# Kernel tuning notes

Measured on AMD Instinct MI355X. Metric: run time of the kernel, lower is better.

Reference implementation:

```python
import jax, jax.numpy as jnp
import numpy as np

N_HEADS = 16
INPUT_DIM = 1024
EMBED_DIM = 1024
KEY_DIM = EMBED_DIM // N_HEADS  # 64, val_dim == key_dim
BATCH = 4
SEQ = 2048


def _uniform(key, shape, bound):
    return jax.random.uniform(key, shape, jnp.float32, -bound, bound)


def setup_inputs() -> dict:
    key = jax.random.key(0)
    kq, k1, k2, k3, k4 = jax.random.split(key, 5)
    stdv_k = 1.0 / np.sqrt(KEY_DIM)
    stdv_e = 1.0 / np.sqrt(EMBED_DIM)
    return {
        "q": jax.random.normal(kq, (BATCH, SEQ, INPUT_DIM), jnp.float32),
        "W_query": _uniform(k1, (N_HEADS, INPUT_DIM, KEY_DIM), stdv_k),
        "W_key": _uniform(k2, (N_HEADS, INPUT_DIM, KEY_DIM), stdv_k),
        "W_val": _uniform(k3, (N_HEADS, INPUT_DIM, KEY_DIM), stdv_k),
        "W_out": _uniform(k4, (N_HEADS, KEY_DIM, EMBED_DIM), stdv_e),
    }


def reference(q, W_query, W_key, W_val, W_out):
    # Self-attention: h = q. Project per head: [H, B, S, dk]
    norm = 1.0 / np.sqrt(KEY_DIM)
    Q = jnp.einsum("bsd,hdk->hbsk", q, W_query)
    K = jnp.einsum("bsd,hdk->hbsk", q, W_key)
    V = jnp.einsum("bsd,hdv->hbsv", q, W_val)
    # compatibility: [H, B, S_q, S_k]
    scores = norm * jnp.einsum("hbqk,hbnk->hbqn", Q, K)
    attn = jax.nn.softmax(scores, axis=-1)
    heads = jnp.einsum("hbqn,hbnv->hbqv", attn, V)
    # combine heads with per-head output projection: [B, S, E]
    out = jnp.einsum("hbqv,hve->bqe", heads, W_out)
    return out
```

## Files before the change

kernel.cpp:

```cpp
#include <hip/hip_runtime.h>
#include <hip/hip_bf16.h>
#include <stdint.h>
#include <math.h>

#define BATCH 4
#define SEQ   2048
#define NHEAD 16
#define DIM   1024
#define DKV   64
#define MTOT  (BATCH*SEQ)

typedef __attribute__((ext_vector_type(8))) short  bf16x8;
typedef __attribute__((ext_vector_type(4))) float  f32x4;
typedef unsigned short u16;
typedef unsigned int   u32;
typedef __attribute__((ext_vector_type(4))) u16 u16x4;
typedef __attribute__((ext_vector_type(2))) u32 u32x2;
typedef __attribute__((ext_vector_type(4))) u32 u32x4;

#define QSCALE 0.18033688011112042f
#define THR    8.0f

__device__ __forceinline__ u16 f2bf(float f) {
  __hip_bfloat16 h = __float2bfloat16(f);
  u16 r;
  __builtin_memcpy(&r, &h, 2);
  return r;
}
__device__ __forceinline__ u32 pkbf(float lo, float hi) {
  __hip_bfloat162 h = __float22bfloat162_rn(float2{lo, hi});
  u32 r;
  __builtin_memcpy(&r, &h, 4);
  return r;
}

__device__ __forceinline__ void gload_lds16(const void* g, void* l) {
  __builtin_amdgcn_global_load_lds((u32 __attribute__((address_space(1)))*)(g),
                                   (u32 __attribute__((address_space(3)))*)(l),
                                   16, 0, 0);
}


__global__ void k_cvt_q(const float* __restrict__ src, u16* __restrict__ dst) {
  const int i = (blockIdx.x * 256 + threadIdx.x) * 4;
  float4 v = *(const float4*)(src + i);
  u32x2 o;
  o[0] = pkbf(v.x, v.y); o[1] = pkbf(v.z, v.w);
  *(u32x2*)(dst + i) = o;
}

__global__ void k_cvt_wproj(const float* __restrict__ w, u16* __restrict__ wt) {
  const int idx = blockIdx.x * 256 + threadIdx.x;
  const int n = idx >> 10, d = idx & 1023;
  wt[idx] = f2bf(w[((n >> 6) << 16) + (d << 6) + (n & 63)]);
}

__global__ void k_cvt_wout(const float* __restrict__ w, u16* __restrict__ wt) {
  const int idx = blockIdx.x * 256 + threadIdx.x;
  const int e = idx >> 10, hv = idx & 1023;
  wt[idx] = f2bf(w[(hv << 10) + e]);
}


template<int MODE>
__device__ __forceinline__ void gemm2(u16* __restrict__ sm,
                                      const u16* __restrict__ A, const u16* __restrict__ Bt,
                                      void* __restrict__ Cp, int m0, int n0) {
  const int tid = threadIdx.x, wid = tid >> 6, lane = tid & 63;
  const int g = lane >> 4, li = lane & 15;
  const int wm = wid >> 1, wn = wid & 1;

  const int c0 = wid * 128 + lane, c1 = c0 + 64;
  const int s0 = (c0 * 8) ^ (((c0 >> 3) & 7) << 3);
  const int s1 = (c1 * 8) ^ (((c1 >> 3) & 7) << 3);
  const int cB = tid;
  const int sB = (cB * 8) ^ (((cB >> 3) & 7) << 3);
  const u16* As0 = A  + (size_t)(m0 + (s0 >> 5)) * DIM + (s0 & 31);
  const u16* As1 = A  + (size_t)(m0 + (s1 >> 5)) * DIM + (s1 & 31);
  const u16* Bs  = Bt + (size_t)(n0 + (sB >> 5)) * DIM + (sB & 31);
  u16* dA0 = sm + wid * 1024;
  u16* dA1 = sm + wid * 1024 + 512;
  u16* dB  = sm + 32768 + wid * 512;

#define SA2(t, ks, tb) do { \
    gload_lds16(As0 + (t) * 64 + (ks) * 32, dA0 + (tb) * 16384 + (ks) * 8192); \
    gload_lds16(As1 + (t) * 64 + (ks) * 32, dA1 + (tb) * 16384 + (ks) * 8192); } while (0)
#define SB2(t, ks, tb) \
    gload_lds16(Bs + (t) * 64 + (ks) * 32, dB + (tb) * 8192 + (ks) * 4096)

  const int vx = ((li >> 1) & 7) << 3;
  const int a_rd = (((wm * 64 + li) * 32) + g * 8) ^ vx;
  const int b_rd = (((wn * 64 + li) * 32) + g * 8) ^ vx;

  f32x4 acc[4][4] = {};

  SA2(0, 0, 0); SB2(0, 0, 0);
  SA2(0, 1, 0); SB2(0, 1, 0);
  SA2(1, 0, 1); SB2(1, 0, 1);
  asm volatile("s_waitcnt vmcnt(6)" ::: "memory");
  __builtin_amdgcn_s_barrier();

#pragma unroll 2
  for (int kt = 0; kt < 16; ++kt) {
    const int cur = kt & 1, t1 = (kt + 1) & 15, t2 = (kt + 2) & 15;
    const u16* pa = sm + cur * 16384 + a_rd;
    const u16* pb = sm + 32768 + cur * 8192 + b_rd;
    bf16x8 af[2], bfq[4];

#pragma unroll
    for (int j = 0; j < 4; ++j) bfq[j] = *(const bf16x8*)(pb + j * 512);
    af[0] = *(const bf16x8*)(pa);
    af[1] = *(const bf16x8*)(pa + 512);
    SA2(t1, 1, cur ^ 1);
    __builtin_amdgcn_s_barrier();
    __builtin_amdgcn_s_setprio(1);
#pragma unroll
    for (int i = 0; i < 2; ++i)
#pragma unroll
      for (int j = 0; j < 4; ++j)
        acc[i][j] = __builtin_amdgcn_mfma_f32_16x16x32_bf16(af[i], bfq[j], acc[i][j], 0, 0, 0);
    __builtin_amdgcn_s_setprio(0);
    __builtin_amdgcn_s_barrier();

    af[0] = *(const bf16x8*)(pa + 2 * 512);
    af[1] = *(const bf16x8*)(pa + 3 * 512);
    SB2(t1, 1, cur ^ 1);
    __builtin_amdgcn_s_barrier();
    __builtin_amdgcn_s_setprio(1);
#pragma unroll
    for (int i = 0; i < 2; ++i)
#pragma unroll
      for (int j = 0; j < 4; ++j)
        acc[i + 2][j] = __builtin_amdgcn_mfma_f32_16x16x32_bf16(af[i], bfq[j], acc[i + 2][j], 0, 0, 0);
    __builtin_amdgcn_s_setprio(0);
    asm volatile("s_waitcnt vmcnt(3)" ::: "memory");
    __builtin_amdgcn_s_barrier();

#pragma unroll
    for (int j = 0; j < 4; ++j) bfq[j] = *(const bf16x8*)(pb + 4096 + j * 512);
    af[0] = *(const bf16x8*)(pa + 8192);
    af[1] = *(const bf16x8*)(pa + 8192 + 512);
    SA2(t2, 0, cur);
    __builtin_amdgcn_s_barrier();
    __builtin_amdgcn_s_setprio(1);
#pragma unroll
    for (int i = 0; i < 2; ++i)
#pragma unroll
      for (int j = 0; j < 4; ++j)
        acc[i][j] = __builtin_amdgcn_mfma_f32_16x16x32_bf16(af[i], bfq[j], acc[i][j], 0, 0, 0);
    __builtin_amdgcn_s_setprio(0);
    __builtin_amdgcn_s_barrier();

    af[0] = *(const bf16x8*)(pa + 8192 + 2 * 512);
    af[1] = *(const bf16x8*)(pa + 8192 + 3 * 512);
    SB2(t2, 0, cur);
    __builtin_amdgcn_s_barrier();
    __builtin_amdgcn_s_setprio(1);
#pragma unroll
    for (int i = 0; i < 2; ++i)
#pragma unroll
      for (int j = 0; j < 4; ++j)
        acc[i + 2][j] = __builtin_amdgcn_mfma_f32_16x16x32_bf16(af[i], bfq[j], acc[i + 2][j], 0, 0, 0);
    __builtin_amdgcn_s_setprio(0);
    asm volatile("s_waitcnt vmcnt(3)" ::: "memory");
    __builtin_amdgcn_s_barrier();
  }
#undef SA2
#undef SB2

#pragma unroll
  for (int i = 0; i < 4; ++i)
#pragma unroll
    for (int j = 0; j < 4; ++j) {
      const int col = n0 + wn * 64 + j * 16 + li;
      if (MODE == 3) {
        const size_t rowb = (size_t)(m0 + wm * 64 + i * 16 + g * 4) + 4 * g - 12 * (i & 1);
        u32x2 w;
        w[0] = pkbf(acc[i][j][0], acc[i][j][1]);
        w[1] = pkbf(acc[i][j][2], acc[i][j][3]);
        *(u32x2*)((u16*)Cp + (size_t)col * MTOT + rowb) = w;
      } else if (MODE == 1) {
#pragma unroll
        for (int r = 0; r < 4; ++r) {
          const size_t row = (size_t)(m0 + wm * 64 + i * 16 + g * 4 + r);
          ((float*)Cp)[row * DIM + col] = acc[i][j][r];
        }
      } else {
#pragma unroll
        for (int r = 0; r < 4; ++r) {
          const size_t row = (size_t)(m0 + wm * 64 + i * 16 + g * 4 + r);
          float v = acc[i][j][r];
          if (MODE == 2) v *= QSCALE;
          ((u16*)Cp)[row * DIM + col] = f2bf(v);
        }
      }
    }
}

__global__ __launch_bounds__(512, 2)
void k_gemm_qkv2(const u16* __restrict__ A, const u16* __restrict__ wq,
                 const u16* __restrict__ wk, const u16* __restrict__ wv,
                 u16* __restrict__ Qo, u16* __restrict__ Ko, u16* __restrict__ Vto) {
  __shared__ u16 sm[49152];
  const int m0 = blockIdx.x * 256;
  const int yt = blockIdx.y;
  const int wsel = yt >> 3;
  const int n0 = (yt & 7) * 128;
  if (wsel == 0)      gemm2<2>(sm, A, wq, Qo,  m0, n0);
  else if (wsel == 1) gemm2<0>(sm, A, wk, Ko,  m0, n0);
  else                gemm2<3>(sm, A, wv, Vto, m0, n0);
}

__global__ __launch_bounds__(512, 2)
void k_gemm_out2(const u16* __restrict__ A, const u16* __restrict__ Bt, float* __restrict__ C) {
  __shared__ u16 sm[49152];
  gemm2<1>(sm, A, Bt, C, blockIdx.x * 256, blockIdx.y * 128);
}


#define KB 64
#define NT (SEQ/KB)

__global__ __launch_bounds__(512, 8)
void k_attn(const u16* __restrict__ Q, const u16* __restrict__ K,
            const u16* __restrict__ Vt, u16* __restrict__ O) {
  const int qt = blockIdx.x, bh = blockIdx.y;
  const int b = bh >> 4, h = bh & 15;
  const int q0 = qt * 128;
  const int tid = threadIdx.x, wid = tid >> 6, lane = tid & 63;
  const int g = lane >> 4, li = lane & 15;

  __shared__ u16 kl[2][KB * 64];
  __shared__ u16 vl[2][KB * 64];

  const size_t rb = (size_t)b * SEQ;
  const int hc = h * DKV;

  bf16x8 qf0, qf1;
  {
    const u16* qp = Q + (rb + q0 + wid * 16 + li) * DIM + hc;
    qf0 = *(const bf16x8*)(qp + g * 8);
    qf1 = *(const bf16x8*)(qp + 32 + g * 8);
  }

  bf16x8 ones;
#pragma unroll
  for (int j = 0; j < 8; ++j) ones[j] = (short)0x3F80;

  float mrun = -1e30f, lrun = 0.f;
  f32x4 o[4] = {};

  const int r8   = lane >> 3;
  const int swz  = ((lane & 7) ^ r8) * 8;
  const int srow = wid * 8 + r8;

  gload_lds16(K  + (rb + srow) * DIM + hc + swz,          &kl[0][wid * 512]);
  gload_lds16(Vt + (size_t)(hc + srow) * MTOT + rb + swz, &vl[0][wid * 512]);

  for (int it = 0; it < NT; ++it) {
    const int cur = it & 1;
    __syncthreads();

    if (it + 1 < NT) {
      const int n1 = (it + 1) * KB;
      gload_lds16(K  + (rb + n1 + srow) * DIM + hc + swz,          &kl[cur ^ 1][wid * 512]);
      gload_lds16(Vt + (size_t)(hc + srow) * MTOT + rb + n1 + swz, &vl[cur ^ 1][wid * 512]);
    }

    const u16* kb = kl[cur];
    const u16* vb = vl[cur];
    const int sw = (li & 7) << 3;

    f32x4 s[4];
    __builtin_amdgcn_s_setprio(1);
#pragma unroll
    for (int t = 0; t < 4; ++t) {
      const int row = t * 16 + li;
      bf16x8 kf0 = *(const bf16x8*)(kb + row * 64 + ((g * 8) ^ sw));
      bf16x8 kf1 = *(const bf16x8*)(kb + row * 64 + ((32 + g * 8) ^ sw));
      f32x4 z = {};
      z = __builtin_amdgcn_mfma_f32_16x16x32_bf16(kf0, qf0, z, 0, 0, 0);
      z = __builtin_amdgcn_mfma_f32_16x16x32_bf16(kf1, qf1, z, 0, 0, 0);
      s[t] = z;
    }
    __builtin_amdgcn_s_setprio(0);

    f32x4 mv = __builtin_elementwise_max(__builtin_elementwise_max(s[0], s[1]),
                                         __builtin_elementwise_max(s[2], s[3]));
    const float lmax = fmaxf(fmaxf(mv[0], mv[1]), fmaxf(mv[2], mv[3]));
    if (__any(lmax - mrun > THR)) {
      float pmax = fmaxf(lmax, __shfl_xor(lmax, 16));
      pmax = fmaxf(pmax, __shfl_xor(pmax, 32));
      const float mn = fmaxf(mrun, pmax);
      const float corr = __builtin_amdgcn_exp2f(mrun - mn);
      mrun = mn;
      lrun *= corr;
#pragma unroll
      for (int t = 0; t < 4; ++t) o[t] *= corr;
    }
    const float mb = mrun;
#pragma unroll
    for (int t = 0; t < 4; ++t)
#pragma unroll
      for (int r = 0; r < 4; ++r)
        s[t][r] = __builtin_amdgcn_exp2f(s[t][r] - mb);

    bf16x8 pa[2];
#pragma unroll
    for (int hh = 0; hh < 2; ++hh) {
      u32x4 pw;
      pw[0] = pkbf(s[2 * hh][0],     s[2 * hh][1]);
      pw[1] = pkbf(s[2 * hh][2],     s[2 * hh][3]);
      pw[2] = pkbf(s[2 * hh + 1][0], s[2 * hh + 1][1]);
      pw[3] = pkbf(s[2 * hh + 1][2], s[2 * hh + 1][3]);
      pa[hh] = __builtin_bit_cast(bf16x8, pw);
    }

    f32x4 zs = {};
    zs = __builtin_amdgcn_mfma_f32_16x16x32_bf16(ones, pa[0], zs, 0, 0, 0);
    zs = __builtin_amdgcn_mfma_f32_16x16x32_bf16(ones, pa[1], zs, 0, 0, 0);

    __builtin_amdgcn_s_setprio(1);
#pragma unroll
    for (int t = 0; t < 4; ++t) {
      const int row = t * 16 + li;
#pragma unroll
      for (int hh = 0; hh < 2; ++hh) {
        bf16x8 vf = *(const bf16x8*)(vb + row * 64 + ((hh * 32 + g * 8) ^ sw));
        o[t] = __builtin_amdgcn_mfma_f32_16x16x32_bf16(vf, pa[hh], o[t], 0, 0, 0);
      }
    }
    __builtin_amdgcn_s_setprio(0);

    lrun += zs[0];
  }

  {
    const float inv = 1.0f / lrun;
    const size_t qrow = rb + q0 + wid * 16 + li;
#pragma unroll
    for (int t = 0; t < 4; ++t) {
      u32x2 w;
      w[0] = pkbf(o[t][0] * inv, o[t][1] * inv);
      w[1] = pkbf(o[t][2] * inv, o[t][3] * inv);
      *(u32x2*)(O + qrow * DIM + hc + t * 16 + 4 * g) = w;
    }
  }
}


extern "C" void kernel_launch(void* const* d_in, const int* in_sizes, int n_in,
                              void* d_out, int out_size, void* d_ws, size_t ws_size,
                              hipStream_t stream) {
  (void)in_sizes; (void)n_in; (void)out_size; (void)ws_size;
  const float* q  = (const float*)d_in[0];
  const float* Wq = (const float*)d_in[1];
  const float* Wk = (const float*)d_in[2];
  const float* Wv = (const float*)d_in[3];
  const float* Wo = (const float*)d_in[4];
  float* out = (float*)d_out;

  char* p = (char*)d_ws;
  u16* qb  = (u16*)p; p += (size_t)MTOT * DIM * 2;
  u16* wqt = (u16*)p; p += (size_t)DIM * DIM * 2;
  u16* wkt = (u16*)p; p += (size_t)DIM * DIM * 2;
  u16* wvt = (u16*)p; p += (size_t)DIM * DIM * 2;
  u16* wot = (u16*)p; p += (size_t)DIM * DIM * 2;
  u16* Qb  = (u16*)p; p += (size_t)MTOT * DIM * 2;
  u16* Kb  = (u16*)p; p += (size_t)MTOT * DIM * 2;
  u16* Vtb = (u16*)p; p += (size_t)MTOT * DIM * 2;
  u16* Hb  = Qb;

  k_cvt_q<<<(MTOT * DIM / 4) / 256, 256, 0, stream>>>(q, qb);
  k_cvt_wproj<<<(DIM * DIM) / 256, 256, 0, stream>>>(Wq, wqt);
  k_cvt_wproj<<<(DIM * DIM) / 256, 256, 0, stream>>>(Wk, wkt);
  k_cvt_wproj<<<(DIM * DIM) / 256, 256, 0, stream>>>(Wv, wvt);
  k_cvt_wout<<<(DIM * DIM) / 256, 256, 0, stream>>>(Wo, wot);

  k_gemm_qkv2<<<dim3(MTOT / 256, 24), 512, 0, stream>>>(qb, wqt, wkt, wvt, Qb, Kb, Vtb);
  k_attn<<<dim3(SEQ / 128, BATCH * NHEAD), 512, 0, stream>>>(Qb, Kb, Vtb, Hb);
  k_gemm_out2<<<dim3(MTOT / 256, DIM / 128), 512, 0, stream>>>(Hb, wot, out);
}
```

Baseline: 217.1 us.

## Rewrite attention kernel with 32x32x16 MFMA tiles and permlane32 P repacking

The attention kernel moves from 16x16x32 MFMAs to 32x32x16 MFMAs. Each wave now handles 32 query rows and each block 256, so the grid is half as large and occupancy is lowered to 4 blocks per CU. The probability tile is rearranged into the PV operand layout with v_permlane32_swap instead of relying on a permuted V layout. The V-transpose store in the QKV GEMM therefore drops its row-permutation offset. The aim is fewer MFMA issues, better K/V reuse per LDS load and less row-max shuffle work, at the cost of more registers per thread and fewer waves in flight.

```diff
diff --git a/kernel.cpp b/kernel.cpp
--- a/kernel.cpp
+++ b/kernel.cpp
@@ -10,11 +10,11 @@
 #define DKV   64
 #define MTOT  (BATCH*SEQ)
 
-typedef __attribute__((ext_vector_type(8))) short  bf16x8;
-typedef __attribute__((ext_vector_type(4))) float  f32x4;
+typedef __attribute__((ext_vector_type(8)))  short bf16x8;
+typedef __attribute__((ext_vector_type(4)))  float f32x4;
+typedef __attribute__((ext_vector_type(16))) float f32x16;
 typedef unsigned short u16;
 typedef unsigned int   u32;
-typedef __attribute__((ext_vector_type(4))) u16 u16x4;
 typedef __attribute__((ext_vector_type(2))) u32 u32x2;
 typedef __attribute__((ext_vector_type(4))) u32 u32x4;
 
@@ -174,7 +174,7 @@
     for (int j = 0; j < 4; ++j) {
       const int col = n0 + wn * 64 + j * 16 + li;
       if (MODE == 3) {
-        const size_t rowb = (size_t)(m0 + wm * 64 + i * 16 + g * 4) + 4 * g - 12 * (i & 1);
+        const size_t rowb = (size_t)(m0 + wm * 64 + i * 16 + g * 4);
         u32x2 w;
         w[0] = pkbf(acc[i][j][0], acc[i][j][1]);
         w[1] = pkbf(acc[i][j][2], acc[i][j][3]);
@@ -218,29 +218,29 @@
 }
 
 
-#define KB 64
-#define NT (SEQ/KB)
-
-__global__ __launch_bounds__(512, 8)
-void k_attn(const u16* __restrict__ Q, const u16* __restrict__ K,
-            const u16* __restrict__ Vt, u16* __restrict__ O) {
+#define NT (SEQ/64)
+
+__global__ __launch_bounds__(512, 4)
+void k_attn32(const u16* __restrict__ Q, const u16* __restrict__ K,
+              const u16* __restrict__ Vt, u16* __restrict__ O) {
   const int qt = blockIdx.x, bh = blockIdx.y;
   const int b = bh >> 4, h = bh & 15;
-  const int q0 = qt * 128;
+  const int q0 = qt * 256;
   const int tid = threadIdx.x, wid = tid >> 6, lane = tid & 63;
-  const int g = lane >> 4, li = lane & 15;
-
-  __shared__ u16 kl[2][KB * 64];
-  __shared__ u16 vl[2][KB * 64];
+  const int ql = lane & 31, hi = lane >> 5;
+
+  __shared__ u16 kl[2][64 * 64];
+  __shared__ u16 vl[2][64 * 64];
 
   const size_t rb = (size_t)b * SEQ;
   const int hc = h * DKV;
-
-  bf16x8 qf0, qf1;
+  const size_t qrow = rb + q0 + wid * 32 + ql;
+
+  bf16x8 qf[4];
   {
-    const u16* qp = Q + (rb + q0 + wid * 16 + li) * DIM + hc;
-    qf0 = *(const bf16x8*)(qp + g * 8);
-    qf1 = *(const bf16x8*)(qp + 32 + g * 8);
+    const u16* qp = Q + qrow * DIM + hc + 8 * hi;
+#pragma unroll
+    for (int ks = 0; ks < 4; ++ks) qf[ks] = *(const bf16x8*)(qp + ks * 16);
   }
 
   bf16x8 ones;
@@ -248,11 +248,12 @@
   for (int j = 0; j < 8; ++j) ones[j] = (short)0x3F80;
 
   float mrun = -1e30f, lrun = 0.f;
-  f32x4 o[4] = {};
+  f32x16 o0 = {}, o1 = {};
 
   const int r8   = lane >> 3;
   const int swz  = ((lane & 7) ^ r8) * 8;
   const int srow = wid * 8 + r8;
+  const int swR  = (ql & 7) << 3;
 
   gload_lds16(K  + (rb + srow) * DIM + hc + swz,          &kl[0][wid * 512]);
   gload_lds16(Vt + (size_t)(hc + srow) * MTOT + rb + swz, &vl[0][wid * 512]);
@@ -262,88 +263,91 @@
     __syncthreads();
 
     if (it + 1 < NT) {
-      const int n1 = (it + 1) * KB;
+      const int n1 = (it + 1) * 64;
       gload_lds16(K  + (rb + n1 + srow) * DIM + hc + swz,          &kl[cur ^ 1][wid * 512]);
       gload_lds16(Vt + (size_t)(hc + srow) * MTOT + rb + n1 + swz, &vl[cur ^ 1][wid * 512]);
     }
 
     const u16* kb = kl[cur];
     const u16* vb = vl[cur];
-    const int sw = (li & 7) << 3;
-
-    f32x4 s[4];
-    __builtin_amdgcn_s_setprio(1);
-#pragma unroll
-    for (int t = 0; t < 4; ++t) {
-      const int row = t * 16 + li;
-      bf16x8 kf0 = *(const bf16x8*)(kb + row * 64 + ((g * 8) ^ sw));
-      bf16x8 kf1 = *(const bf16x8*)(kb + row * 64 + ((32 + g * 8) ^ sw));
-      f32x4 z = {};
-      z = __builtin_amdgcn_mfma_f32_16x16x32_bf16(kf0, qf0, z, 0, 0, 0);
-      z = __builtin_amdgcn_mfma_f32_16x16x32_bf16(kf1, qf1, z, 0, 0, 0);
-      s[t] = z;
-    }
-    __builtin_amdgcn_s_setprio(0);
-
-    f32x4 mv = __builtin_elementwise_max(__builtin_elementwise_max(s[0], s[1]),
-                                         __builtin_elementwise_max(s[2], s[3]));
-    const float lmax = fmaxf(fmaxf(mv[0], mv[1]), fmaxf(mv[2], mv[3]));
+
+    f32x16 s0 = {}, s1 = {};
+    __builtin_amdgcn_s_setprio(1);
+#pragma unroll
+    for (int ks = 0; ks < 4; ++ks) {
+      const int co = (ks * 16 + 8 * hi) ^ swR;
+      bf16x8 kf0 = *(const bf16x8*)(kb + ql * 64 + co);
+      bf16x8 kf1 = *(const bf16x8*)(kb + (ql + 32) * 64 + co);
+      s0 = __builtin_amdgcn_mfma_f32_32x32x16_bf16(kf0, qf[ks], s0, 0, 0, 0);
+      s1 = __builtin_amdgcn_mfma_f32_32x32x16_bf16(kf1, qf[ks], s1, 0, 0, 0);
+    }
+    __builtin_amdgcn_s_setprio(0);
+
+    f32x16 mm = __builtin_elementwise_max(s0, s1);
+    float a0 = fmaxf(fmaxf(mm[0], mm[1]),  fmaxf(mm[2], mm[3]));
+    float a1 = fmaxf(fmaxf(mm[4], mm[5]),  fmaxf(mm[6], mm[7]));
+    float a2 = fmaxf(fmaxf(mm[8], mm[9]),  fmaxf(mm[10], mm[11]));
+    float a3 = fmaxf(fmaxf(mm[12], mm[13]), fmaxf(mm[14], mm[15]));
+    const float lmax = fmaxf(fmaxf(a0, a1), fmaxf(a2, a3));
     if (__any(lmax - mrun > THR)) {
-      float pmax = fmaxf(lmax, __shfl_xor(lmax, 16));
-      pmax = fmaxf(pmax, __shfl_xor(pmax, 32));
+      const float pmax = fmaxf(lmax, __shfl_xor(lmax, 32));
       const float mn = fmaxf(mrun, pmax);
       const float corr = __builtin_amdgcn_exp2f(mrun - mn);
       mrun = mn;
       lrun *= corr;
-#pragma unroll
-      for (int t = 0; t < 4; ++t) o[t] *= corr;
+      o0 *= corr;
+      o1 *= corr;
     }
     const float mb = mrun;
 #pragma unroll
-    for (int t = 0; t < 4; ++t)
-#pragma unroll
-      for (int r = 0; r < 4; ++r)
-        s[t][r] = __builtin_amdgcn_exp2f(s[t][r] - mb);
-
-    bf16x8 pa[2];
-#pragma unroll
-    for (int hh = 0; hh < 2; ++hh) {
-      u32x4 pw;
-      pw[0] = pkbf(s[2 * hh][0],     s[2 * hh][1]);
-      pw[1] = pkbf(s[2 * hh][2],     s[2 * hh][3]);
-      pw[2] = pkbf(s[2 * hh + 1][0], s[2 * hh + 1][1]);
-      pw[3] = pkbf(s[2 * hh + 1][2], s[2 * hh + 1][3]);
-      pa[hh] = __builtin_bit_cast(bf16x8, pw);
-    }
-
-    f32x4 zs = {};
-    zs = __builtin_amdgcn_mfma_f32_16x16x32_bf16(ones, pa[0], zs, 0, 0, 0);
-    zs = __builtin_amdgcn_mfma_f32_16x16x32_bf16(ones, pa[1], zs, 0, 0, 0);
-
-    __builtin_amdgcn_s_setprio(1);
-#pragma unroll
-    for (int t = 0; t < 4; ++t) {
-      const int row = t * 16 + li;
-#pragma unroll
-      for (int hh = 0; hh < 2; ++hh) {
-        bf16x8 vf = *(const bf16x8*)(vb + row * 64 + ((hh * 32 + g * 8) ^ sw));
-        o[t] = __builtin_amdgcn_mfma_f32_16x16x32_bf16(vf, pa[hh], o[t], 0, 0, 0);
-      }
-    }
-    __builtin_amdgcn_s_setprio(0);
-
-    lrun += zs[0];
+    for (int r = 0; r < 16; ++r) {
+      s0[r] = __builtin_amdgcn_exp2f(s0[r] - mb);
+      s1[r] = __builtin_amdgcn_exp2f(s1[r] - mb);
+    }
+
+    f32x16 zacc = {};
+#define PVGRP(SV, TT)                                                         \
+    {                                                                         \
+      _Pragma("unroll")                                                       \
+      for (int bs = 0; bs < 2; ++bs) {                                        \
+        u32 Aw  = pkbf(SV[8 * bs + 0], SV[8 * bs + 1]);                       \
+        u32 Axw = pkbf(SV[8 * bs + 2], SV[8 * bs + 3]);                       \
+        u32 Cw  = pkbf(SV[8 * bs + 4], SV[8 * bs + 5]);                       \
+        u32 Cxw = pkbf(SV[8 * bs + 6], SV[8 * bs + 7]);                       \
+        asm("v_permlane32_swap_b32 %0, %1" : "+v"(Aw), "+v"(Cw));             \
+        asm("v_permlane32_swap_b32 %0, %1" : "+v"(Axw), "+v"(Cxw));           \
+        u32x4 pw; pw[0] = Aw; pw[1] = Axw; pw[2] = Cw; pw[3] = Cxw;           \
+        bf16x8 W = __builtin_bit_cast(bf16x8, pw);                            \
+        const int kvo = (((TT) * 2 + bs) * 16 + 8 * hi) ^ swR;                \
+        bf16x8 va = *(const bf16x8*)(vb + ql * 64 + kvo);                     \
+        bf16x8 vc = *(const bf16x8*)(vb + (ql + 32) * 64 + kvo);              \
+        zacc = __builtin_amdgcn_mfma_f32_32x32x16_bf16(ones, W, zacc, 0, 0, 0); \
+        o0   = __builtin_amdgcn_mfma_f32_32x32x16_bf16(va,  W, o0,  0, 0, 0); \
+        o1   = __builtin_amdgcn_mfma_f32_32x32x16_bf16(vc,  W, o1,  0, 0, 0); \
+      }                                                                       \
+    }
+    __builtin_amdgcn_s_setprio(1);
+    PVGRP(s0, 0)
+    PVGRP(s1, 1)
+    __builtin_amdgcn_s_setprio(0);
+#undef PVGRP
+
+    lrun += zacc[0];
   }
 
   {
     const float inv = 1.0f / lrun;
-    const size_t qrow = rb + q0 + wid * 16 + li;
-#pragma unroll
-    for (int t = 0; t < 4; ++t) {
+    u16* Ob = O + qrow * DIM + hc + 4 * hi;
+#pragma unroll
+    for (int a = 0; a < 4; ++a) {
       u32x2 w;
-      w[0] = pkbf(o[t][0] * inv, o[t][1] * inv);
-      w[1] = pkbf(o[t][2] * inv, o[t][3] * inv);
-      *(u32x2*)(O + qrow * DIM + hc + t * 16 + 4 * g) = w;
+      w[0] = pkbf(o0[4 * a + 0] * inv, o0[4 * a + 1] * inv);
+      w[1] = pkbf(o0[4 * a + 2] * inv, o0[4 * a + 3] * inv);
+      *(u32x2*)(Ob + 8 * a) = w;
+      u32x2 w2;
+      w2[0] = pkbf(o1[4 * a + 0] * inv, o1[4 * a + 1] * inv);
+      w2[1] = pkbf(o1[4 * a + 2] * inv, o1[4 * a + 3] * inv);
+      *(u32x2*)(Ob + 32 + 8 * a) = w2;
     }
   }
 }
@@ -378,6 +382,6 @@
   k_cvt_wout<<<(DIM * DIM) / 256, 256, 0, stream>>>(Wo, wot);
 
   k_gemm_qkv2<<<dim3(MTOT / 256, 24), 512, 0, stream>>>(qb, wqt, wkt, wvt, Qb, Kb, Vtb);
-  k_attn<<<dim3(SEQ / 128, BATCH * NHEAD), 512, 0, stream>>>(Qb, Kb, Vtb, Hb);
+  k_attn32<<<dim3(SEQ / 256, BATCH * NHEAD), 512, 0, stream>>>(Qb, Kb, Vtb, Hb);
   k_gemm_out2<<<dim3(MTOT / 256, DIM / 128), 512, 0, stream>>>(Hb, wot, out);
 }
```

New measurement: 219.0 us. About the same (+0.9%).
